# Kernel optimization log

Hardware: AMD Instinct MI355X
Metric: run time of the kernel (lower is better)

Reference implementation:

```python
import jax, jax.numpy as jnp
import numpy as np

# Real spherical harmonics for l=0,1,2 in 'component' normalization (sqrt(4*pi) * Y_std),
# m ordered -l..l per l, matching the e3nn Kernel's norm_Y = sqrt(4*pi)*I convention.
_SQ3 = 3.0 ** 0.5
_SQ5 = 5.0 ** 0.5
_SQ15 = 15.0 ** 0.5

def sph_harm_012(d):
    # d: [N,3] unit directions -> Y: [N,9]
    x, y, z = d[:, 0], d[:, 1], d[:, 2]
    one = jnp.ones_like(x)
    return jnp.stack([
        one,                      # l=0
        _SQ3 * y,                 # l=1, m=-1
        _SQ3 * z,                 # l=1, m=0
        _SQ3 * x,                 # l=1, m=1
        _SQ15 * x * y,            # l=2, m=-2
        _SQ15 * y * z,            # l=2, m=-1
        0.5 * _SQ5 * (3.0 * z * z - 1.0),  # l=2, m=0
        _SQ15 * x * z,            # l=2, m=1
        0.5 * _SQ15 * (x * x - y * y),     # l=2, m=2
    ], axis=1)


def setup_inputs() -> dict:
    key = jax.random.key(0)
    ks = jax.random.split(key, 7)
    N, I, J, Y, W, H = 65536, 16, 16, 9, 96, 128
    return {
        "r": jax.random.normal(ks[0], (N, 3), dtype=jnp.float32),
        "Q": jax.random.normal(ks[1], (I, J, Y, W), dtype=jnp.float32) * 0.1,
        "W1": jax.random.normal(ks[2], (1, H), dtype=jnp.float32),
        "b1": jax.random.normal(ks[3], (H,), dtype=jnp.float32),
        "W2": jax.random.normal(ks[4], (H, W), dtype=jnp.float32) * (1.0 / H ** 0.5),
        "b2": jax.random.normal(ks[5], (W,), dtype=jnp.float32),
        "K0": jax.random.normal(ks[6], (I, J), dtype=jnp.float32),
    }


def reference(r, Q, W1, b1, W2, b2, K0):
    R_EPS = 0.0
    radii = jnp.linalg.norm(r, axis=1)              # [N]
    mask = radii > R_EPS                            # [N]
    safe = jnp.where(mask, radii, 1.0)
    d = r / safe[:, None]                           # unit directions [N,3]
    Ysh = sph_harm_012(d)                           # [N,9]
    # Radial MLP: R -> R^w
    h = jax.nn.relu(radii[:, None] * W1[0][None, :] + b1)  # [N,H]
    Rad = h @ W2 + b2                               # [N,96]
    # kernel1 = einsum('ijyw,zy,zw->zij', Q, Y, R)
    k1 = jnp.einsum('ijyw,zy,zw->zij', Q, Ysh, Rad, optimize=True)  # [N,16,16]
    # scatter-by-mask: points at/below r_eps get the self-interaction kernel K0
    return jnp.where(mask[:, None, None], k1, K0[None, :, :])
```

## Files before the change

### kernel.cpp

```cpp
#include <hip/hip_runtime.h>
#include <hip/hip_bf16.h>


typedef __attribute__((ext_vector_type(8))) short bfrag;
typedef __attribute__((ext_vector_type(4))) float fx4;

#define WS_AT   512
#define WS_BT   50048
#define WS_QT   99584
#define WS_IVZ  2213120
#define WS_PERM 2344192
#define WS_BH   2606336
#define WS_BTAB 2673920
#define NCHUNKS 1153
#define NQTBLK  1161

__device__ inline unsigned short f2bf(float f) {
  union { float f; unsigned int u; } v; v.f = f;
  unsigned int r = v.u + 0x7FFFu + ((v.u >> 16) & 1u);
  return (unsigned short)(r >> 16);
}
__device__ inline unsigned int pack2(float a, float b) {
  return (unsigned int)f2bf(a) | ((unsigned int)f2bf(b) << 16);
}
__device__ inline void gl_lds16(const void* g, void* l) {
  __builtin_amdgcn_global_load_lds(
      (const __attribute__((address_space(1))) unsigned int*)g,
      (__attribute__((address_space(3))) unsigned int*)l, 16, 0, 0);
}

__global__ void k_pre(const float* __restrict__ W1, const float* __restrict__ b1,
                      const float* __restrict__ W2, const float* __restrict__ b2,
                      const float* __restrict__ r,
                      float* __restrict__ At, float* __restrict__ Bt,
                      unsigned short* __restrict__ ivz,
                      unsigned short* __restrict__ bh) {
  const int tid = threadIdx.x;
  const float INF = __builtin_inff();

  if (blockIdx.x == 256) {
    __shared__ float w2_s[128 * 96];
    __shared__ float val_s[128], stb_s[128], w1_s[128], b1_s[128];
    __shared__ int   perm_s[128];
    for (int i = tid; i < 128 * 96; i += 256) w2_s[i] = W2[i];
    if (tid < 128) {
      float w1 = W1[tid], b1v = b1[tid];
      w1_s[tid] = w1; b1_s[tid] = b1v;
      float tj = -b1v / w1;
      bool valid = (w1 != 0.0f) && (tj > 0.0f);
      val_s[tid] = valid ? tj : INF;
    }
    __syncthreads();
    if (tid < 128) {
      float v = val_s[tid];
      int rank = 0;
      for (int m = 0; m < 128; ++m) {
        float vm = val_s[m];
        rank += (vm < v || (vm == v && m < tid)) ? 1 : 0;
      }
      stb_s[rank] = v; perm_s[rank] = tid;
    }
    __syncthreads();
    if (tid < 96) {
      float s0  = stb_s[0];
      float tm0 = (s0 == INF) ? 1.0f : 0.5f * s0;
      float sa = 0.f, sb = 0.f;
#pragma unroll 8
      for (int j = 0; j < 128; ++j) {
        float on = (tm0 * w1_s[j] + b1_s[j] > 0.0f) ? 1.f : 0.f;
        float w2 = on * w2_s[j * 96 + tid];
        sa += w2 * w1_s[j]; sb += w2 * b1_s[j];
      }
      float b2v = b2[tid];
      At[tid] = sa; Bt[tid] = sb + b2v;
#pragma unroll 8
      for (int s = 0; s < 128; ++s) {
        int   j    = perm_s[s];
        float live = (stb_s[s] < INF) ? 1.f : 0.f;
        float sgn  = (w1_s[j] > 0.f) ? live : -live;
        float w2   = sgn * w2_s[j * 96 + tid];
        sa += w2 * w1_s[j]; sb += w2 * b1_s[j];
        At[(s + 1) * 96 + tid] = sa; Bt[(s + 1) * 96 + tid] = sb + b2v;
      }
    }
    return;
  }

  __shared__ float tj_s[128];
  __shared__ unsigned int h_s[129];
  const int bb = blockIdx.x;
  if (tid < 128) {
    float w1 = W1[tid], b1v = b1[tid];
    float tj = -b1v / w1;
    bool valid = (w1 != 0.0f) && (tj > 0.0f);
    tj_s[tid] = valid ? tj : INF;
  }
  if (tid < 129) h_s[tid] = 0;
  __syncthreads();
  const int z = bb * 256 + tid;
  float rx = r[z * 3 + 0], ry = r[z * 3 + 1], rz = r[z * 3 + 2];
  float rad = sqrtf(rx * rx + ry * ry + rz * rz);
  int cnt = 0;
#pragma unroll 16
  for (int j = 0; j < 128; ++j) cnt += (tj_s[j] < rad) ? 1 : 0;
  ivz[z] = (unsigned short)(cnt | (rad > 0.f ? 0 : 0x8000));
  atomicAdd(&h_s[cnt], 1u);
  __syncthreads();
  if (tid < 129) bh[bb * 132 + tid] = (unsigned short)h_s[tid];
}

__global__ void k_mid(const float* __restrict__ Q, const float* __restrict__ At,
                      const float* __restrict__ Bt,
                      const unsigned short* __restrict__ ivz,
                      const unsigned short* __restrict__ bh,
                      unsigned short* __restrict__ qt,
                      unsigned int* __restrict__ perm,
                      uint4* __restrict__ btab) {
  const int tid = threadIdx.x;
  if (blockIdx.x < NQTBLK) {
    __shared__ float at_s[96], bt_s[96];
    const int iv = blockIdx.x % 129, y = blockIdx.x / 129, c = tid;
    if (c < 96) { at_s[c] = At[iv * 96 + c]; bt_s[c] = Bt[iv * 96 + c]; }
    __syncthreads();
    const float* q = Q + (size_t)c * 864 + y * 96;
    float qa = 0.f, qb = 0.f;
#pragma unroll
    for (int w4 = 0; w4 < 24; ++w4) {
      float4 qv = *(const float4*)(q + w4 * 4);
      qa += qv.x * at_s[w4*4+0] + qv.y * at_s[w4*4+1] + qv.z * at_s[w4*4+2] + qv.w * at_s[w4*4+3];
      qb += qv.x * bt_s[w4*4+0] + qv.y * bt_s[w4*4+1] + qv.z * bt_s[w4*4+2] + qv.w * bt_s[w4*4+3];
    }
    char* base = (char*)qt + (size_t)iv * 16384 + (c >> 4) * 1024 + (c & 15) * 16;
    const int ka = y, kb = 9 + y;
    *(unsigned short*)(base + (ka >> 3) * 256 + (ka & 7) * 2) = f2bf(qa);
    *(unsigned short*)(base + (kb >> 3) * 256 + (kb & 7) * 2) = f2bf(qb);
    if (y == 0) {
#pragma unroll
      for (int k = 18; k < 32; ++k)
        *(unsigned short*)(base + (k >> 3) * 256 + (k & 7) * 2) = 0;
    }
    return;
  }
  __shared__ unsigned int tot_s[129], pre_s[129], st_s[130], eo_s[130];
  __shared__ unsigned int cur_s[129];
  const int bb = blockIdx.x - NQTBLK;
  if (tid < 129) {
    unsigned tot = 0, pre = 0;
#pragma unroll 8
    for (int b = 0; b < 256; ++b) {
      unsigned v = bh[b * 132 + tid];
      tot += v;
      pre += (b < bb) ? v : 0;
    }
    tot_s[tid] = tot; pre_s[tid] = pre;
  }
  __syncthreads();
  if (tid == 0) {
    unsigned s = 0, e = 0;
    for (int i = 0; i < 129; ++i) {
      st_s[i] = s; eo_s[i] = e;
      s += tot_s[i]; e += (tot_s[i] + 63) >> 6;
    }
    st_s[129] = s; eo_s[129] = e;
  }
  __syncthreads();
  if (tid < 129) cur_s[tid] = st_s[tid] + pre_s[tid];
  __syncthreads();
  const int z = bb * 256 + tid;
  unsigned u = ivz[z];
  unsigned iv = u & 255u;
  unsigned pos = atomicAdd(&cur_s[iv], 1u);
  perm[pos] = (unsigned)z | ((u & 0x8000u) << 16);
  if (bb == 0) {
    const unsigned total = eo_s[129];
    for (unsigned e = tid; e < NCHUNKS; e += 256) {
      uint4 ent = make_uint4(0, 0, 0, 0);
      if (e < total) {
        int lo = 0, hi = 128;
        while (lo < hi) { int mid = (lo + hi + 1) >> 1;
                          if (eo_s[mid] <= e) lo = mid; else hi = mid - 1; }
        unsigned chunk = e - eo_s[lo];
        unsigned cnt = tot_s[lo] - chunk * 64; if (cnt > 64) cnt = 64;
        ent = make_uint4((unsigned)lo, st_s[lo] + chunk * 64, cnt, 0);
      }
      btab[e] = ent;
    }
  }
}

__global__ __launch_bounds__(256)
void k_out(const float* __restrict__ r, const unsigned short* __restrict__ qt,
           const unsigned int* __restrict__ perm, const uint4* __restrict__ btab,
           const float* __restrict__ K0, float* __restrict__ out) {
  __shared__ unsigned short T_s[8192];
  __shared__ unsigned short coef_s[2048];
  __shared__ unsigned int z_s[64];
  __shared__ unsigned int mk_s[64];

  const uint4 ent = btab[blockIdx.x];
  const unsigned iv = ent.x, base = ent.y, cnt = ent.z;
  if (cnt == 0) return;

  const int tid  = threadIdx.x;
  const int lane = tid & 63;
  const int wave = tid >> 6;
  const int lg   = lane >> 4;
  const int l15  = lane & 15;

  {
    const char* src = (const char*)qt + (size_t)iv * 16384 + wave * 1024 + lane * 16;
    char* dst = (char*)T_s + wave * 1024;
#pragma unroll
    for (int i = 0; i < 4; ++i) gl_lds16(src + i * 4096, dst + i * 4096);
  }

  if (tid < 64) {
    const int j = tid;
    unsigned pz = perm[base + (j < (int)cnt ? j : 0)];
    unsigned z = pz & 0x7FFFFFFFu;
    z_s[j] = z; mk_s[j] = pz >> 31;
    const float* rg = r + (size_t)z * 3;
    float rx = rg[0], ry = rg[1], rz = rg[2];
    float rad = sqrtf(rx * rx + ry * ry + rz * rz);
    float inv = (rad > 0.f) ? (1.0f / rad) : 1.0f;
    float x = rx * inv, y = ry * inv, zc = rz * inv;
    const float SQ3 = 1.7320508075688772f, SQ5 = 2.2360679774997896f,
                SQ15 = 3.872983346207417f;
    float ys[9];
    ys[0] = 1.f;
    ys[1] = SQ3 * y;  ys[2] = SQ3 * zc;  ys[3] = SQ3 * x;
    ys[4] = SQ15 * x * y;  ys[5] = SQ15 * y * zc;
    ys[6] = 0.5f * SQ5 * (3.f * zc * zc - 1.f);
    ys[7] = SQ15 * x * zc;
    ys[8] = 0.5f * SQ15 * (x * x - y * y);
    float cf[18];
#pragma unroll
    for (int m = 0; m < 9; ++m) { cf[m] = ys[m] * rad; cf[9 + m] = ys[m]; }
    char* cbp = (char*)coef_s + (j >> 4) * 1024 + (j & 15) * 16;
#pragma unroll
    for (int g = 0; g < 4; ++g)
#pragma unroll
      for (int p = 0; p < 4; ++p) {
        const int k0 = g * 8 + p * 2, k1 = k0 + 1;
        float v0 = (k0 < 18) ? cf[k0] : 0.f;
        float v1 = (k1 < 18) ? cf[k1] : 0.f;
        *(unsigned int*)(cbp + g * 256 + p * 4) = pack2(v0, v1);
      }
  }
  __syncthreads();

  fx4 acc[16];
#pragma unroll
  for (int cb2 = 0; cb2 < 16; ++cb2)
#pragma unroll
    for (int e = 0; e < 4; ++e) acc[cb2][e] = 0.f;

  const bfrag a = *(const bfrag*)((char*)coef_s + wave * 1024 + lg * 256 + l15 * 16);
#pragma unroll
  for (int cb2 = 0; cb2 < 16; ++cb2) {
    const bfrag b = *(const bfrag*)((char*)T_s + cb2 * 1024 + lg * 256 + l15 * 16);
    acc[cb2] = __builtin_amdgcn_mfma_f32_16x16x32_bf16(a, b, acc[cb2], 0, 0, 0);
  }

  float k0v[16];
#pragma unroll
  for (int cb2 = 0; cb2 < 16; ++cb2) k0v[cb2] = K0[cb2 * 16 + l15];
#pragma unroll
  for (int q = 0; q < 4; ++q) {
    const int br = wave * 16 + lg * 4 + q;
    if (br < (int)cnt) {
      const unsigned z = z_s[br];
      const bool mq = mk_s[br] != 0;
      float* ob = out + (size_t)z * 256 + l15;
#pragma unroll
      for (int cb2 = 0; cb2 < 16; ++cb2)
        ob[cb2 * 16] = mq ? k0v[cb2] : acc[cb2][q];
    }
  }
}

extern "C" void kernel_launch(void* const* d_in, const int* in_sizes, int n_in,
                              void* d_out, int out_size, void* d_ws, size_t ws_size,
                              hipStream_t stream) {
  const float* r  = (const float*)d_in[0];
  const float* Q  = (const float*)d_in[1];
  const float* W1 = (const float*)d_in[2];
  const float* b1 = (const float*)d_in[3];
  const float* W2 = (const float*)d_in[4];
  const float* b2 = (const float*)d_in[5];
  const float* K0 = (const float*)d_in[6];
  float* out = (float*)d_out;
  char* ws = (char*)d_ws;
  float* At = (float*)(ws + WS_AT);
  float* Bt = (float*)(ws + WS_BT);
  unsigned short* qt  = (unsigned short*)(ws + WS_QT);
  unsigned short* ivz = (unsigned short*)(ws + WS_IVZ);
  unsigned int* permb = (unsigned int*)(ws + WS_PERM);
  unsigned short* bh  = (unsigned short*)(ws + WS_BH);
  uint4* btab         = (uint4*)(ws + WS_BTAB);

  hipLaunchKernelGGL(k_pre, dim3(257), dim3(256), 0, stream,
                     W1, b1, W2, b2, r, At, Bt, ivz, bh);
  hipLaunchKernelGGL(k_mid, dim3(NQTBLK + 256), dim3(256), 0, stream,
                     Q, At, Bt, ivz, bh, qt, permb, btab);
  hipLaunchKernelGGL(k_out, dim3(NCHUNKS), dim3(256), 0, stream,
                     r, qt, permb, btab, K0, out);
}
```

Baseline: 62.60 us.

## Parallelize radial table over interval blocks and stage Q rows through LDS

New measurement: 60.17 us. -3.9%, faster.

```diff
diff --git a/kernel.cpp b/kernel.cpp
--- a/kernel.cpp
+++ b/kernel.cpp
@@ -38,11 +38,9 @@
   const int tid = threadIdx.x;
   const float INF = __builtin_inff();
 
-  if (blockIdx.x == 256) {
-    __shared__ float w2_s[128 * 96];
-    __shared__ float val_s[128], stb_s[128], w1_s[128], b1_s[128];
-    __shared__ int   perm_s[128];
-    for (int i = tid; i < 128 * 96; i += 256) w2_s[i] = W2[i];
+  if (blockIdx.x >= 256) {
+    const int tiv = blockIdx.x - 256;
+    __shared__ float w1_s[128], b1_s[128], val_s[128], stb_s[128];
     if (tid < 128) {
       float w1 = W1[tid], b1v = b1[tid];
       w1_s[tid] = w1; b1_s[tid] = b1v;
@@ -58,30 +56,24 @@
         float vm = val_s[m];
         rank += (vm < v || (vm == v && m < tid)) ? 1 : 0;
       }
-      stb_s[rank] = v; perm_s[rank] = tid;
+      stb_s[rank] = v;
     }
     __syncthreads();
     if (tid < 96) {
-      float s0  = stb_s[0];
-      float tm0 = (s0 == INF) ? 1.0f : 0.5f * s0;
+      float lo_e = (tiv == 0) ? 0.f : stb_s[tiv - 1];
+      float hi_e = (tiv < 128) ? stb_s[tiv] : INF;
+      float tstar;
+      if (lo_e < INF) tstar = (hi_e < INF) ? 0.5f * (lo_e + hi_e) : (lo_e + 1.0f);
+      else            tstar = 0.f;
       float sa = 0.f, sb = 0.f;
 #pragma unroll 8
       for (int j = 0; j < 128; ++j) {
-        float on = (tm0 * w1_s[j] + b1_s[j] > 0.0f) ? 1.f : 0.f;
-        float w2 = on * w2_s[j * 96 + tid];
+        float on = (w1_s[j] * tstar + b1_s[j] > 0.0f) ? 1.f : 0.f;
+        float w2 = on * W2[j * 96 + tid];
         sa += w2 * w1_s[j]; sb += w2 * b1_s[j];
       }
-      float b2v = b2[tid];
-      At[tid] = sa; Bt[tid] = sb + b2v;
-#pragma unroll 8
-      for (int s = 0; s < 128; ++s) {
-        int   j    = perm_s[s];
-        float live = (stb_s[s] < INF) ? 1.f : 0.f;
-        float sgn  = (w1_s[j] > 0.f) ? live : -live;
-        float w2   = sgn * w2_s[j * 96 + tid];
-        sa += w2 * w1_s[j]; sb += w2 * b1_s[j];
-        At[(s + 1) * 96 + tid] = sa; Bt[(s + 1) * 96 + tid] = sb + b2v;
-      }
+      At[tiv * 96 + tid] = sa;
+      Bt[tiv * 96 + tid] = sb + b2[tid];
     }
     return;
   }
@@ -109,40 +101,61 @@
   if (tid < 129) bh[bb * 132 + tid] = (unsigned short)h_s[tid];
 }
 
-__global__ void k_mid(const float* __restrict__ Q, const float* __restrict__ At,
-                      const float* __restrict__ Bt,
-                      const unsigned short* __restrict__ ivz,
-                      const unsigned short* __restrict__ bh,
-                      unsigned short* __restrict__ qt,
-                      unsigned int* __restrict__ perm,
-                      uint4* __restrict__ btab) {
+__global__ __launch_bounds__(256)
+void k_mid(const float* __restrict__ Q, const float* __restrict__ At,
+           const float* __restrict__ Bt,
+           const unsigned short* __restrict__ ivz,
+           const unsigned short* __restrict__ bh,
+           unsigned short* __restrict__ qt,
+           unsigned int* __restrict__ perm,
+           uint4* __restrict__ btab) {
+  __shared__ float smem[12800];
   const int tid = threadIdx.x;
+
   if (blockIdx.x < NQTBLK) {
-    __shared__ float at_s[96], bt_s[96];
-    const int iv = blockIdx.x % 129, y = blockIdx.x / 129, c = tid;
-    if (c < 96) { at_s[c] = At[iv * 96 + c]; bt_s[c] = Bt[iv * 96 + c]; }
-    __syncthreads();
-    const float* q = Q + (size_t)c * 864 + y * 96;
-    float qa = 0.f, qb = 0.f;
-#pragma unroll
-    for (int w4 = 0; w4 < 24; ++w4) {
-      float4 qv = *(const float4*)(q + w4 * 4);
-      qa += qv.x * at_s[w4*4+0] + qv.y * at_s[w4*4+1] + qv.z * at_s[w4*4+2] + qv.w * at_s[w4*4+3];
-      qb += qv.x * bt_s[w4*4+0] + qv.y * bt_s[w4*4+1] + qv.z * bt_s[w4*4+2] + qv.w * bt_s[w4*4+3];
-    }
-    char* base = (char*)qt + (size_t)iv * 16384 + (c >> 4) * 1024 + (c & 15) * 16;
-    const int ka = y, kb = 9 + y;
-    *(unsigned short*)(base + (ka >> 3) * 256 + (ka & 7) * 2) = f2bf(qa);
-    *(unsigned short*)(base + (kb >> 3) * 256 + (kb & 7) * 2) = f2bf(qb);
-    if (y == 0) {
-#pragma unroll
-      for (int k = 18; k < 32; ++k)
-        *(unsigned short*)(base + (k >> 3) * 256 + (k & 7) * 2) = 0;
+    float* qs   = smem;
+    float* at_s = smem + 128 * 97;
+    float* bt_s = at_s + 96;
+    const int iv = blockIdx.x % 129, y = blockIdx.x / 129;
+    if (tid < 96) { at_s[tid] = At[iv * 96 + tid]; bt_s[tid] = Bt[iv * 96 + tid]; }
+#pragma unroll
+    for (int half = 0; half < 2; ++half) {
+      __syncthreads();
+      for (int i = tid; i < 128 * 24; i += 256) {
+        const int c_loc = i / 24, f4 = i - c_loc * 24;
+        float4 v = *(const float4*)(Q + (size_t)(half * 128 + c_loc) * 864 + y * 96 + f4 * 4);
+        float* d = qs + c_loc * 97 + f4 * 4;
+        d[0] = v.x; d[1] = v.y; d[2] = v.z; d[3] = v.w;
+      }
+      __syncthreads();
+      if (tid < 128) {
+        const int c = half * 128 + tid;
+        const float* row = qs + tid * 97;
+        float qa = 0.f, qb = 0.f;
+#pragma unroll 8
+        for (int w = 0; w < 96; ++w) {
+          float qv = row[w];
+          qa += qv * at_s[w]; qb += qv * bt_s[w];
+        }
+        char* base = (char*)qt + (size_t)iv * 16384 + (c >> 4) * 1024 + (c & 15) * 16;
+        const int ka = y, kb = 9 + y;
+        *(unsigned short*)(base + (ka >> 3) * 256 + (ka & 7) * 2) = f2bf(qa);
+        *(unsigned short*)(base + (kb >> 3) * 256 + (kb & 7) * 2) = f2bf(qb);
+        if (y == 0) {
+#pragma unroll
+          for (int k = 18; k < 32; ++k)
+            *(unsigned short*)(base + (k >> 3) * 256 + (k & 7) * 2) = 0;
+        }
+      }
     }
     return;
   }
-  __shared__ unsigned int tot_s[129], pre_s[129], st_s[130], eo_s[130];
-  __shared__ unsigned int cur_s[129];
+
+  unsigned int* tot_s = (unsigned int*)smem;
+  unsigned int* pre_s = tot_s + 129;
+  unsigned int* st_s  = pre_s + 129;
+  unsigned int* eo_s  = st_s + 130;
+  unsigned int* cur_s = eo_s + 130;
   const int bb = blockIdx.x - NQTBLK;
   if (tid < 129) {
     unsigned tot = 0, pre = 0;
@@ -207,6 +220,9 @@
   const int lg   = lane >> 4;
   const int l15  = lane & 15;
 
+  unsigned pz = 0;
+  if (tid < 64) pz = perm[base + (tid < (int)cnt ? tid : 0)];
+
   {
     const char* src = (const char*)qt + (size_t)iv * 16384 + wave * 1024 + lane * 16;
     char* dst = (char*)T_s + wave * 1024;
@@ -216,7 +232,6 @@
 
   if (tid < 64) {
     const int j = tid;
-    unsigned pz = perm[base + (j < (int)cnt ? j : 0)];
     unsigned z = pz & 0x7FFFFFFFu;
     z_s[j] = z; mk_s[j] = pz >> 31;
     const float* rg = r + (size_t)z * 3;
@@ -299,7 +314,7 @@
   unsigned short* bh  = (unsigned short*)(ws + WS_BH);
   uint4* btab         = (uint4*)(ws + WS_BTAB);
 
-  hipLaunchKernelGGL(k_pre, dim3(257), dim3(256), 0, stream,
+  hipLaunchKernelGGL(k_pre, dim3(385), dim3(256), 0, stream,
                      W1, b1, W2, b2, r, At, Bt, ivz, bh);
   hipLaunchKernelGGL(k_mid, dim3(NQTBLK + 256), dim3(256), 0, stream,
                      Q, At, Bt, ivz, bh, qt, permb, btab);
```
